# Performance work log

Hardware: AMD Instinct MI355X
Metric: run time of the kernel (lower is better)

Reference implementation:

```python
import jax, jax.numpy as jnp
import numpy as np

B, T, V, E, H, C = 32, 512, 50000, 300, 1024, 2


def setup_inputs() -> dict:
    key = jax.random.key(0)
    ks = jax.random.split(key, 24)
    def w(k, shape):
        return jax.random.normal(k, shape, jnp.float32) * 0.05
    inp = {
        "padded_texts": jax.random.randint(ks[0], (B, T), 0, V),
        "lengths": jax.random.randint(ks[1], (B,), 1, T + 1),
        "emb": w(ks[2], (V, E)),
    }
    i = 3
    for layer, din in ((0, E), (1, 2 * H)):
        for d in ("f", "b"):
            inp[f"w_ih_l{layer}{d}"] = w(ks[i], (4 * H, din)); i += 1
            inp[f"w_hh_l{layer}{d}"] = w(ks[i], (4 * H, H)); i += 1
            inp[f"b_ih_l{layer}{d}"] = w(ks[i], (4 * H,)); i += 1
            inp[f"b_hh_l{layer}{d}"] = w(ks[i], (4 * H,)); i += 1
    inp["lin_w"] = w(ks[i], (C, 2 * H))
    inp["lin_b"] = w(ks[i + 1], (C,))
    return inp


def _reverse_padded(x, lengths):
    # Reverse each sequence within its valid length (pad tail clipped to idx 0;
    # those positions are masked out downstream anyway).
    Tt = x.shape[1]
    idx = jnp.clip(lengths[:, None] - 1 - jnp.arange(Tt)[None, :], 0)
    return jnp.take_along_axis(x, idx[:, :, None], axis=1)


def _run_dir(x, mask, W_ih, W_hh, b_ih, b_hh):
    # x: [B,T,D], mask: [B,T] bool. Returns ([B,T,H] outputs, [B,H] last hidden).
    Bb = x.shape[0]
    Hh = W_hh.shape[1]
    xp = jnp.einsum('btd,gd->btg', x, W_ih) + b_ih + b_hh  # [B,T,4H]
    def step(carry, inp):
        h, c = carry
        g_in, m = inp
        gates = g_in + h @ W_hh.T
        i, f, g, o = jnp.split(gates, 4, axis=-1)  # torch gate order i,f,g,o
        c_new = jax.nn.sigmoid(f) * c + jax.nn.sigmoid(i) * jnp.tanh(g)
        h_new = jax.nn.sigmoid(o) * jnp.tanh(c_new)
        m = m[:, None]
        h = jnp.where(m, h_new, h)
        c = jnp.where(m, c_new, c)
        return (h, c), h
    h0 = jnp.zeros((Bb, Hh), x.dtype)
    (hT, _), outs = jax.lax.scan(step, (h0, h0), (xp.swapaxes(0, 1), mask.T))
    return outs.swapaxes(0, 1), hT


def _bilstm_layer(x, lengths, mask, pf, pb):
    out_f, h_f = _run_dir(x, mask, *pf)
    xr = _reverse_padded(x, lengths)
    out_br, h_b = _run_dir(xr, mask, *pb)
    out_b = _reverse_padded(out_br, lengths)
    return jnp.concatenate([out_f, out_b], -1), h_f, h_b


def reference(padded_texts, lengths, emb,
              w_ih_l0f, w_hh_l0f, b_ih_l0f, b_hh_l0f,
              w_ih_l0b, w_hh_l0b, b_ih_l0b, b_hh_l0b,
              w_ih_l1f, w_hh_l1f, b_ih_l1f, b_hh_l1f,
              w_ih_l1b, w_hh_l1b, b_ih_l1b, b_hh_l1b,
              lin_w, lin_b):
    x = emb[padded_texts]  # [B,T,E]
    mask = jnp.arange(x.shape[1])[None, :] < lengths[:, None]
    x1, _, _ = _bilstm_layer(x, lengths, mask,
                             (w_ih_l0f, w_hh_l0f, b_ih_l0f, b_hh_l0f),
                             (w_ih_l0b, w_hh_l0b, b_ih_l0b, b_hh_l0b))
    _, h2f, h2b = _bilstm_layer(x1, lengths, mask,
                                (w_ih_l1f, w_hh_l1f, b_ih_l1f, b_hh_l1f),
                                (w_ih_l1b, w_hh_l1b, b_ih_l1b, b_hh_l1b))
    # torch: hn[-1] = layer-2 backward, hn[-2] = layer-2 forward;
    # source concatenates (hn[-1], hn[-2]) -> (backward, forward).
    concat = jnp.concatenate([h2b, h2f], axis=1)  # [B,2H]
    return concat @ lin_w.T + lin_b  # [B,2]
```

## Files before the change

### kernel.cpp

```cpp
#include <hip/hip_runtime.h>
#include <hip/hip_bf16.h>
#include <math.h>

typedef __bf16 bf16_8 __attribute__((ext_vector_type(8)));
typedef float  f32x4  __attribute__((ext_vector_type(4)));
typedef unsigned u32x4 __attribute__((ext_vector_type(4)));

#define B_   32
#define T_   512
#define H_   1024
#define G_   4096
#define E_   300
#define EP_  320
#define CT_  128
#define NCH  4

constexpr size_t OFF_HBUF  = 0;
constexpr size_t SZ_ZERO   = 1048576;
constexpr size_t OFF_CBUF  = SZ_ZERO;
constexpr size_t OFF_H2F   = OFF_CBUF + 262144;
constexpr size_t OFF_H2B   = OFF_H2F + 65536;
constexpr size_t OFF_W0F   = OFF_H2B + 65536;
constexpr size_t OFF_W0B   = OFF_W0F + 2621440;
constexpr size_t OFF_W1F   = OFF_W0B + 2621440;
constexpr size_t OFF_W1B   = OFF_W1F + 16777216;
constexpr size_t OFF_EMB   = OFF_W1B + 16777216;
constexpr size_t OFF_OUTF  = OFF_EMB + 32000000;
constexpr size_t OFF_OUTB  = OFF_OUTF + 33554432;
constexpr size_t OFF_XPF   = OFF_OUTB + 33554432;
constexpr size_t OFF_XPB   = OFF_XPF + 33554432;
constexpr size_t WS_NEED   = OFF_XPB + 33554432;

#define WSTR 1032
constexpr int LDS_W  = 0;
constexpr int LDS_H  = 32 * WSTR * 2;
constexpr int LDS_G  = LDS_H + 32 * WSTR * 2;
constexpr int LDS_C  = LDS_G + 32 * 36 * 4;
constexpr int LDS_L  = LDS_C + 32 * 8 * 4;
constexpr int SMEM_REC = LDS_L + 128;

__device__ __forceinline__ float sigf(float x) { return 1.f / (1.f + __expf(-x)); }

__device__ __forceinline__ bf16_8 cvt8(f32x4 lo, f32x4 hi) {
    bf16_8 v;
    #pragma unroll
    for (int e = 0; e < 4; ++e) { v[e] = (__bf16)lo[e]; v[4 + e] = (__bf16)hi[e]; }
    return v;
}

__global__ void pad_w0(const float* __restrict__ wf, const float* __restrict__ wb,
                       __bf16* __restrict__ of, __bf16* __restrict__ ob) {
    int r = blockIdx.x, dir = blockIdx.y, k = threadIdx.x;
    const float* s = dir ? wb : wf;
    __bf16* d = (dir ? ob : of) + (size_t)r * EP_;
    d[k] = (k < E_) ? (__bf16)s[(size_t)r * E_ + k] : (__bf16)0.f;
}

__global__ void cvt_w1(const float* __restrict__ wf, const float* __restrict__ wb,
                       __bf16* __restrict__ of, __bf16* __restrict__ ob) {
    int n = blockIdx.x;
    const float* s = (blockIdx.y ? wb : wf) + (size_t)n * 2048;
    __bf16* d = (blockIdx.y ? ob : of) + (size_t)n * 2048;
    for (int k = threadIdx.x; k < 2048; k += 256) d[k] = (__bf16)s[k];
}

__global__ void cvt_emb(const float* __restrict__ emb, __bf16* __restrict__ embp) {
    int v = blockIdx.x, k = threadIdx.x;
    embp[(size_t)v * EP_ + k] = (k < E_) ? (__bf16)emb[(size_t)v * E_ + k] : (__bf16)0.f;
}

__global__ __launch_bounds__(256) void gemm_l0c(
    const int* __restrict__ texts, const int* __restrict__ lens,
    const __bf16* __restrict__ embp, const __bf16* __restrict__ W,
    const float* __restrict__ bih, const float* __restrict__ bhh,
    __bf16* __restrict__ D, int dir, int t0) {
    constexpr int LDT = 40;
    __shared__ __bf16 As[128 * LDT];
    __shared__ __bf16 Bs[128 * LDT];
    int m0 = (blockIdx.x >> 5) * 128, n0 = (blockIdx.x & 31) * 128;
    int tid = threadIdx.x;
    int rr = tid >> 2, c8 = (tid & 3) * 8;
    const __bf16* pA[2]; const __bf16* pB[2];
    #pragma unroll
    for (int s = 0; s < 2; ++s) {
        int row = m0 + rr + s * 64;
        int b = row >> 7, t = t0 + (row & 127);
        int tt = t;
        if (dir) { int L = lens[b]; tt = L - 1 - t; if (tt < 0) tt = 0; }
        pA[s] = embp + (size_t)texts[b * T_ + tt] * EP_;
        pB[s] = W + (size_t)(n0 + rr + s * 64) * EP_;
    }
    int lane = tid & 63, wid = tid >> 6;
    int wm = (wid >> 1) * 64, wn = (wid & 1) * 64;
    int row16 = lane & 15, quad = lane >> 4;
    bf16_8 apf[2], bpf[2];
    #pragma unroll
    for (int s = 0; s < 2; ++s) {
        apf[s] = *(const bf16_8*)(pA[s] + c8);
        bpf[s] = *(const bf16_8*)(pB[s] + c8);
    }
    f32x4 acc[4][4] = {};
    for (int k0 = 0; k0 < EP_; k0 += 32) {
        #pragma unroll
        for (int s = 0; s < 2; ++s) {
            *(bf16_8*)&As[(rr + s * 64) * LDT + c8] = apf[s];
            *(bf16_8*)&Bs[(rr + s * 64) * LDT + c8] = bpf[s];
        }
        __syncthreads();
        if (k0 + 32 < EP_) {
            int k8 = k0 + 32 + c8;
            #pragma unroll
            for (int s = 0; s < 2; ++s) {
                apf[s] = *(const bf16_8*)(pA[s] + k8);
                bpf[s] = *(const bf16_8*)(pB[s] + k8);
            }
        }
        bf16_8 a[4], b[4];
        #pragma unroll
        for (int i = 0; i < 4; ++i) a[i] = *(const bf16_8*)&As[(wm + i * 16 + row16) * LDT + quad * 8];
        #pragma unroll
        for (int j = 0; j < 4; ++j) b[j] = *(const bf16_8*)&Bs[(wn + j * 16 + row16) * LDT + quad * 8];
        #pragma unroll
        for (int i = 0; i < 4; ++i)
            #pragma unroll
            for (int j = 0; j < 4; ++j)
                acc[i][j] = __builtin_amdgcn_mfma_f32_16x16x32_bf16(a[i], b[j], acc[i][j], 0, 0, 0);
        __syncthreads();
    }
    #pragma unroll
    for (int j = 0; j < 4; ++j) {
        int col = n0 + wn + j * 16 + row16;
        float bias = bih[col] + bhh[col];
        #pragma unroll
        for (int i = 0; i < 4; ++i) {
            int rowb = m0 + wm + i * 16 + quad * 4;
            #pragma unroll
            for (int r = 0; r < 4; ++r)
                D[(size_t)(rowb + r) * G_ + col] = (__bf16)(acc[i][j][r] + bias);
        }
    }
}

__global__ __launch_bounds__(256) void gemm_l1c(
    const __bf16* __restrict__ outf, const __bf16* __restrict__ outbr,
    const int* __restrict__ lens, const __bf16* __restrict__ W,
    const float* __restrict__ bih, const float* __restrict__ bhh,
    __bf16* __restrict__ D, int dir, int t0) {
    constexpr int LDT = 40;
    __shared__ __bf16 As[128 * LDT];
    __shared__ __bf16 Bs[128 * LDT];
    int m0 = (blockIdx.x >> 5) * 128, n0 = (blockIdx.x & 31) * 128;
    int tid = threadIdx.x;
    int rr = tid >> 2, c8 = (tid & 3) * 8;
    const __bf16* pLo[2]; const __bf16* pHi[2]; const __bf16* pB[2];
    #pragma unroll
    for (int s = 0; s < 2; ++s) {
        int row = m0 + rr + s * 64;
        int b = row >> 7, t = t0 + (row & 127);
        int L = lens[b];
        int rev = L - 1 - t; if (rev < 0) rev = 0;
        int tf = dir ? rev : t;
        int tb = dir ? t : rev;
        pLo[s] = outf  + ((size_t)b * T_ + tf) * H_;
        pHi[s] = outbr + ((size_t)b * T_ + tb) * H_;
        pB[s]  = W + (size_t)(n0 + rr + s * 64) * (2 * H_);
    }
    int lane = tid & 63, wid = tid >> 6;
    int wm = (wid >> 1) * 64, wn = (wid & 1) * 64;
    int row16 = lane & 15, quad = lane >> 4;
    bf16_8 apf[2], bpf[2];
    #pragma unroll
    for (int s = 0; s < 2; ++s) {
        apf[s] = *(const bf16_8*)(pLo[s] + c8);
        bpf[s] = *(const bf16_8*)(pB[s] + c8);
    }
    f32x4 acc[4][4] = {};
    for (int k0 = 0; k0 < 2 * H_; k0 += 32) {
        #pragma unroll
        for (int s = 0; s < 2; ++s) {
            *(bf16_8*)&As[(rr + s * 64) * LDT + c8] = apf[s];
            *(bf16_8*)&Bs[(rr + s * 64) * LDT + c8] = bpf[s];
        }
        __syncthreads();
        if (k0 + 32 < 2 * H_) {
            int k8 = k0 + 32 + c8;
            #pragma unroll
            for (int s = 0; s < 2; ++s) {
                const __bf16* src = (k8 < H_) ? pLo[s] + k8 : pHi[s] + (k8 - H_);
                apf[s] = *(const bf16_8*)src;
                bpf[s] = *(const bf16_8*)&pB[s][k8];
            }
        }
        bf16_8 a[4], b[4];
        #pragma unroll
        for (int i = 0; i < 4; ++i) a[i] = *(const bf16_8*)&As[(wm + i * 16 + row16) * LDT + quad * 8];
        #pragma unroll
        for (int j = 0; j < 4; ++j) b[j] = *(const bf16_8*)&Bs[(wn + j * 16 + row16) * LDT + quad * 8];
        #pragma unroll
        for (int i = 0; i < 4; ++i)
            #pragma unroll
            for (int j = 0; j < 4; ++j)
                acc[i][j] = __builtin_amdgcn_mfma_f32_16x16x32_bf16(a[i], b[j], acc[i][j], 0, 0, 0);
        __syncthreads();
    }
    #pragma unroll
    for (int j = 0; j < 4; ++j) {
        int col = n0 + wn + j * 16 + row16;
        float bias = bih[col] + bhh[col];
        #pragma unroll
        for (int i = 0; i < 4; ++i) {
            int rowb = m0 + wm + i * 16 + quad * 4;
            #pragma unroll
            for (int r = 0; r < 4; ++r)
                D[(size_t)(rowb + r) * G_ + col] = (__bf16)(acc[i][j][r] + bias);
        }
    }
}

__global__ __launch_bounds__(256) void lstm_rec(
    const __bf16* __restrict__ xp_f, const __bf16* __restrict__ xp_b,
    const float* __restrict__ whh_f, const float* __restrict__ whh_b,
    const int* __restrict__ lens,
    unsigned* __restrict__ hbuf,
    float* __restrict__ cbuf,
    __bf16* __restrict__ out_f, __bf16* __restrict__ out_b,
    int t0, int seq) {
    extern __shared__ char smem[];
    __bf16* Wl = (__bf16*)(smem + LDS_W);
    __bf16* Hl = (__bf16*)(smem + LDS_H);
    float*  Gl = (float*)(smem + LDS_G);
    float*  Cl = (float*)(smem + LDS_C);
    int*    Ll = (int*)(smem + LDS_L);

    int blk = blockIdx.x;
    int dir = blk >> 7;
    int myb = blk & 127;
    int j0  = myb * 8;
    int tid = threadIdx.x;
    const __bf16* xp  = dir ? xp_b : xp_f;
    const float*  whh = dir ? whh_b : whh_f;
    __bf16* outp = dir ? out_b : out_f;

    int em = tid >> 3, eu = tid & 7;
    int src  = tid & 127;
    int half = tid >> 7;

    for (int i = tid; i < 32 * 128; i += 256) {
        int n = i >> 7, k8 = (i & 127) * 8;
        int grow = (n >> 3) * H_ + j0 + (n & 7);
        f32x4 lo = *(const f32x4*)&whh[(size_t)grow * H_ + k8];
        f32x4 hi = *(const f32x4*)&whh[(size_t)grow * H_ + k8 + 4];
        *(bf16_8*)&Wl[n * WSTR + k8] = cvt8(lo, hi);
    }
    if (tid < 32) Ll[tid] = lens[tid];
    Cl[tid] = (t0 == 0) ? 0.f : cbuf[dir * (B_ * H_) + em * H_ + j0 + eu];
    __syncthreads();

    int lane = tid & 63, wid = tid >> 6;
    int row16 = lane & 15, quad = lane >> 4;
    int m0 = (wid >> 1) * 16, n0 = (wid & 1) * 16;
    int tend = t0 + CT_;

    for (int t = t0; t < tend; ++t) {
        size_t xbase = ((size_t)em * CT_ + (t - t0)) * G_ + j0 + eu;
        __bf16 xg0 = xp[xbase];
        __bf16 xg1 = xp[xbase + H_];
        __bf16 xg2 = xp[xbase + 2 * H_];
        __bf16 xg3 = xp[xbase + 3 * H_];

        const unsigned* hs32 = hbuf + (size_t)((t & 1) * 2 + dir) * (B_ * H_);
        unsigned t16 = (unsigned)t << 16;
        u32x4 tv; tv[0] = t16; tv[1] = t16; tv[2] = t16; tv[3] = t16;
        #pragma unroll 1
        for (int g = 0; g < 2; ++g) {
            u32x4 hv[16];
            while (true) {
                #pragma unroll
                for (int s = 0; s < 8; ++s) {
                    const unsigned* p = hs32 + (half + 2 * (g * 8 + s)) * H_ + src * 8;
                    asm volatile("global_load_dwordx4 %0, %1, off sc0 sc1"
                                 : "=v"(hv[2 * s]) : "v"(p));
                    asm volatile("global_load_dwordx4 %0, %1, off sc0 sc1"
                                 : "=v"(hv[2 * s + 1]) : "v"(p + 4));
                }
                asm volatile("s_waitcnt vmcnt(0)" ::: "memory");
                __builtin_amdgcn_sched_barrier(0);
                u32x4 x = hv[0] ^ tv;
                #pragma unroll
                for (int s = 1; s < 16; ++s) x |= (hv[s] ^ tv);
                if (((x[0] | x[1] | x[2] | x[3]) & 0xffff0000u) == 0) break;
            }
            #pragma unroll
            for (int s = 0; s < 8; ++s) {
                u32x4 lo = hv[2 * s], hi = hv[2 * s + 1], pk;
                pk[0] = (lo[0] & 0xffffu) | (lo[1] << 16);
                pk[1] = (lo[2] & 0xffffu) | (lo[3] << 16);
                pk[2] = (hi[0] & 0xffffu) | (hi[1] << 16);
                pk[3] = (hi[2] & 0xffffu) | (hi[3] << 16);
                *(u32x4*)&Hl[(half + 2 * (g * 8 + s)) * WSTR + src * 8] = pk;
            }
        }
        __syncthreads();
        f32x4 acc0 = {0.f, 0.f, 0.f, 0.f}, acc1 = {0.f, 0.f, 0.f, 0.f};
        #pragma unroll
        for (int kc = 0; kc < 32; kc += 2) {
            bf16_8 a0 = *(const bf16_8*)&Hl[(m0 + row16) * WSTR + kc * 32 + quad * 8];
            bf16_8 b0 = *(const bf16_8*)&Wl[(n0 + row16) * WSTR + kc * 32 + quad * 8];
            acc0 = __builtin_amdgcn_mfma_f32_16x16x32_bf16(a0, b0, acc0, 0, 0, 0);
            bf16_8 a1 = *(const bf16_8*)&Hl[(m0 + row16) * WSTR + (kc + 1) * 32 + quad * 8];
            bf16_8 b1 = *(const bf16_8*)&Wl[(n0 + row16) * WSTR + (kc + 1) * 32 + quad * 8];
            acc1 = __builtin_amdgcn_mfma_f32_16x16x32_bf16(a1, b1, acc1, 0, 0, 0);
        }
        #pragma unroll
        for (int r = 0; r < 4; ++r)
            Gl[(m0 + quad * 4 + r) * 36 + n0 + row16] = acc0[r] + acc1[r];
        __syncthreads();
        {
            float pi = Gl[em * 36 + eu]      + (float)xg0;
            float pf = Gl[em * 36 + 8 + eu]  + (float)xg1;
            float pg = Gl[em * 36 + 16 + eu] + (float)xg2;
            float po = Gl[em * 36 + 24 + eu] + (float)xg3;
            float co = Cl[tid];
            float cn = sigf(pf) * co + sigf(pi) * tanhf(pg);
            float hn = sigf(po) * tanhf(cn);
            __bf16 heff;
            if (t < Ll[em]) { Cl[tid] = cn; heff = (__bf16)hn; }
            else            { heff = Hl[em * WSTR + j0 + eu]; }
            {
                unsigned* hp = hbuf + (size_t)(((t + 1) & 1) * 2 + dir) * (B_ * H_)
                             + em * H_ + j0 + eu;
                unsigned hv32 = ((unsigned)(t + 1) << 16)
                              | (unsigned)*(const unsigned short*)&heff;
                asm volatile("global_store_dword %0, %1, off sc0 sc1"
                             :: "v"(hp), "v"(hv32) : "memory");
            }
            if (seq)              outp[((size_t)em * T_ + t) * H_ + j0 + eu] = heff;
            else if (t == T_ - 1) outp[(size_t)em * H_ + j0 + eu] = heff;
        }
        __syncthreads();
    }
    cbuf[dir * (B_ * H_) + em * H_ + j0 + eu] = Cl[tid];
}

__global__ void final_linear(const __bf16* __restrict__ h2f, const __bf16* __restrict__ h2b,
                             const float* __restrict__ lin_w, const float* __restrict__ lin_b,
                             float* __restrict__ out) {
    __shared__ float red[4];
    int b = blockIdx.x >> 1, c = blockIdx.x & 1;
    int tid = threadIdx.x;
    const __bf16* hb = h2b + (size_t)b * H_;
    const __bf16* hf = h2f + (size_t)b * H_;
    const float* w = lin_w + (size_t)c * (2 * H_);
    float s = 0.f;
    for (int j = tid; j < H_; j += 256)
        s += (float)hb[j] * w[j] + (float)hf[j] * w[H_ + j];
    for (int off = 32; off; off >>= 1) s += __shfl_down(s, off, 64);
    if ((tid & 63) == 0) red[tid >> 6] = s;
    __syncthreads();
    if (tid == 0)
        out[b * 2 + c] = red[0] + red[1] + red[2] + red[3] + lin_b[c];
}

extern "C" void kernel_launch(void* const* d_in, const int* in_sizes, int n_in,
                              void* d_out, int out_size, void* d_ws, size_t ws_size,
                              hipStream_t stream) {
    const int*   texts = (const int*)d_in[0];
    const int*   lens  = (const int*)d_in[1];
    const float* emb   = (const float*)d_in[2];
    const float* wih0f = (const float*)d_in[3];
    const float* whh0f = (const float*)d_in[4];
    const float* bih0f = (const float*)d_in[5];
    const float* bhh0f = (const float*)d_in[6];
    const float* wih0b = (const float*)d_in[7];
    const float* whh0b = (const float*)d_in[8];
    const float* bih0b = (const float*)d_in[9];
    const float* bhh0b = (const float*)d_in[10];
    const float* wih1f = (const float*)d_in[11];
    const float* whh1f = (const float*)d_in[12];
    const float* bih1f = (const float*)d_in[13];
    const float* bhh1f = (const float*)d_in[14];
    const float* wih1b = (const float*)d_in[15];
    const float* whh1b = (const float*)d_in[16];
    const float* bih1b = (const float*)d_in[17];
    const float* bhh1b = (const float*)d_in[18];
    const float* linw  = (const float*)d_in[19];
    const float* linb  = (const float*)d_in[20];

    char* ws = (char*)d_ws;
    unsigned* hbuf  = (unsigned*)(ws + OFF_HBUF);
    float*    cbuf  = (float*)(ws + OFF_CBUF);
    __bf16*   h2f   = (__bf16*)(ws + OFF_H2F);
    __bf16*   h2b   = (__bf16*)(ws + OFF_H2B);
    __bf16*   w0f   = (__bf16*)(ws + OFF_W0F);
    __bf16*   w0b   = (__bf16*)(ws + OFF_W0B);
    __bf16*   w1f   = (__bf16*)(ws + OFF_W1F);
    __bf16*   w1b   = (__bf16*)(ws + OFF_W1B);
    __bf16*   embp  = (__bf16*)(ws + OFF_EMB);
    __bf16*   outf  = (__bf16*)(ws + OFF_OUTF);
    __bf16*   outbr = (__bf16*)(ws + OFF_OUTB);
    __bf16*   xpf   = (__bf16*)(ws + OFF_XPF);
    __bf16*   xpb   = (__bf16*)(ws + OFF_XPB);

    if (ws_size < WS_NEED) return;

    hipMemsetAsync(ws, 0, SZ_ZERO, stream);
    hipFuncSetAttribute((const void*)lstm_rec, hipFuncAttributeMaxDynamicSharedMemorySize, SMEM_REC);

    pad_w0 <<<dim3(G_, 2), 320, 0, stream>>>(wih0f, wih0b, w0f, w0b);
    cvt_w1 <<<dim3(G_, 2), 256, 0, stream>>>(wih1f, wih1b, w1f, w1b);
    cvt_emb<<<50000, 320, 0, stream>>>(emb, embp);

    unsigned* hb0 = hbuf;
    unsigned* hb1 = hbuf + 131072;

    for (int c = 0; c < NCH; ++c) {
        int t0 = c * CT_;
        gemm_l0c<<<1024, 256, 0, stream>>>(texts, lens, embp, w0f, bih0f, bhh0f, xpf, 0, t0);
        gemm_l0c<<<1024, 256, 0, stream>>>(texts, lens, embp, w0b, bih0b, bhh0b, xpb, 1, t0);
        lstm_rec<<<256, 256, SMEM_REC, stream>>>(xpf, xpb, whh0f, whh0b, lens,
                                                 hb0, cbuf, outf, outbr, t0, 1);
    }
    for (int c = 0; c < NCH; ++c) {
        int t0 = c * CT_;
        gemm_l1c<<<1024, 256, 0, stream>>>(outf, outbr, lens, w1f, bih1f, bhh1f, xpf, 0, t0);
        gemm_l1c<<<1024, 256, 0, stream>>>(outf, outbr, lens, w1b, bih1b, bhh1b, xpb, 1, t0);
        lstm_rec<<<256, 256, SMEM_REC, stream>>>(xpf, xpb, whh1f, whh1b, lens,
                                                 hb1, cbuf, h2f, h2b, t0, 0);
    }
    final_linear<<<B_ * 2, 256, 0, stream>>>(h2f, h2b, linw, linb, (float*)d_out);
}
```

Baseline: 6.903 ms.

## Interleave gate columns in xp layout and retry only stale h-buffer chunks

The input-projection GEMMs now write their outputs with the four gate columns of each hidden unit interleaved. This lets the recurrent kernel fetch all four gate preactivations with a single 8-byte vector load per step instead of four scattered 2-byte loads. The h-buffer spin-wait now keeps a per-chunk pending mask, reloading and repacking only chunks whose timestamp tag is still stale rather than re-reading all sixteen vectors on every retry. This reduces memory traffic on the serial critical path, at the cost of a more branchy polling loop.

```diff
diff --git a/kernel.cpp b/kernel.cpp
--- a/kernel.cpp
+++ b/kernel.cpp
@@ -3,6 +3,7 @@
 #include <math.h>
 
 typedef __bf16 bf16_8 __attribute__((ext_vector_type(8)));
+typedef __bf16 bf16_4 __attribute__((ext_vector_type(4)));
 typedef float  f32x4  __attribute__((ext_vector_type(4)));
 typedef unsigned u32x4 __attribute__((ext_vector_type(4)));
 
@@ -131,12 +132,13 @@
     for (int j = 0; j < 4; ++j) {
         int col = n0 + wn + j * 16 + row16;
         float bias = bih[col] + bhh[col];
+        int nc = (col & 1023) * 4 + (col >> 10);
         #pragma unroll
         for (int i = 0; i < 4; ++i) {
             int rowb = m0 + wm + i * 16 + quad * 4;
             #pragma unroll
             for (int r = 0; r < 4; ++r)
-                D[(size_t)(rowb + r) * G_ + col] = (__bf16)(acc[i][j][r] + bias);
+                D[(size_t)(rowb + r) * G_ + nc] = (__bf16)(acc[i][j][r] + bias);
         }
     }
 }
@@ -207,12 +209,13 @@
     for (int j = 0; j < 4; ++j) {
         int col = n0 + wn + j * 16 + row16;
         float bias = bih[col] + bhh[col];
+        int nc = (col & 1023) * 4 + (col >> 10);
         #pragma unroll
         for (int i = 0; i < 4; ++i) {
             int rowb = m0 + wm + i * 16 + quad * 4;
             #pragma unroll
             for (int r = 0; r < 4; ++r)
-                D[(size_t)(rowb + r) * G_ + col] = (__bf16)(acc[i][j][r] + bias);
+                D[(size_t)(rowb + r) * G_ + nc] = (__bf16)(acc[i][j][r] + bias);
         }
     }
 }
@@ -262,43 +265,47 @@
     int tend = t0 + CT_;
 
     for (int t = t0; t < tend; ++t) {
-        size_t xbase = ((size_t)em * CT_ + (t - t0)) * G_ + j0 + eu;
-        __bf16 xg0 = xp[xbase];
-        __bf16 xg1 = xp[xbase + H_];
-        __bf16 xg2 = xp[xbase + 2 * H_];
-        __bf16 xg3 = xp[xbase + 3 * H_];
+        bf16_4 xg = *(const bf16_4*)&xp[((size_t)em * CT_ + (t - t0)) * G_ + (size_t)(j0 + eu) * 4];
 
         const unsigned* hs32 = hbuf + (size_t)((t & 1) * 2 + dir) * (B_ * H_);
         unsigned t16 = (unsigned)t << 16;
-        u32x4 tv; tv[0] = t16; tv[1] = t16; tv[2] = t16; tv[3] = t16;
         #pragma unroll 1
         for (int g = 0; g < 2; ++g) {
             u32x4 hv[16];
-            while (true) {
+            unsigned pend = 0xffu;
+            #pragma unroll 1
+            do {
                 #pragma unroll
-                for (int s = 0; s < 8; ++s) {
-                    const unsigned* p = hs32 + (half + 2 * (g * 8 + s)) * H_ + src * 8;
-                    asm volatile("global_load_dwordx4 %0, %1, off sc0 sc1"
-                                 : "=v"(hv[2 * s]) : "v"(p));
-                    asm volatile("global_load_dwordx4 %0, %1, off sc0 sc1"
-                                 : "=v"(hv[2 * s + 1]) : "v"(p + 4));
+                for (int s2 = 0; s2 < 8; ++s2) {
+                    if (pend & (1u << s2)) {
+                        const unsigned* p = hs32 + (half + 2 * (g * 8 + s2)) * H_ + src * 8;
+                        asm volatile("global_load_dwordx4 %0, %1, off sc0 sc1"
+                                     : "=v"(hv[2 * s2]) : "v"(p));
+                        asm volatile("global_load_dwordx4 %0, %1, off sc0 sc1"
+                                     : "=v"(hv[2 * s2 + 1]) : "v"(p + 4));
+                    }
                 }
                 asm volatile("s_waitcnt vmcnt(0)" ::: "memory");
                 __builtin_amdgcn_sched_barrier(0);
-                u32x4 x = hv[0] ^ tv;
                 #pragma unroll
-                for (int s = 1; s < 16; ++s) x |= (hv[s] ^ tv);
-                if (((x[0] | x[1] | x[2] | x[3]) & 0xffff0000u) == 0) break;
-            }
-            #pragma unroll
-            for (int s = 0; s < 8; ++s) {
-                u32x4 lo = hv[2 * s], hi = hv[2 * s + 1], pk;
-                pk[0] = (lo[0] & 0xffffu) | (lo[1] << 16);
-                pk[1] = (lo[2] & 0xffffu) | (lo[3] << 16);
-                pk[2] = (hi[0] & 0xffffu) | (hi[1] << 16);
-                pk[3] = (hi[2] & 0xffffu) | (hi[3] << 16);
-                *(u32x4*)&Hl[(half + 2 * (g * 8 + s)) * WSTR + src * 8] = pk;
-            }
+                for (int s2 = 0; s2 < 8; ++s2) {
+                    if (pend & (1u << s2)) {
+                        u32x4 lo = hv[2 * s2], hi = hv[2 * s2 + 1];
+                        unsigned bad = ((lo[0] ^ t16) | (lo[1] ^ t16) | (lo[2] ^ t16) | (lo[3] ^ t16)
+                                      | (hi[0] ^ t16) | (hi[1] ^ t16) | (hi[2] ^ t16) | (hi[3] ^ t16))
+                                      & 0xffff0000u;
+                        if (!bad) {
+                            u32x4 pk;
+                            pk[0] = (lo[0] & 0xffffu) | (lo[1] << 16);
+                            pk[1] = (lo[2] & 0xffffu) | (lo[3] << 16);
+                            pk[2] = (hi[0] & 0xffffu) | (hi[1] << 16);
+                            pk[3] = (hi[2] & 0xffffu) | (hi[3] << 16);
+                            *(u32x4*)&Hl[(half + 2 * (g * 8 + s2)) * WSTR + src * 8] = pk;
+                            pend &= ~(1u << s2);
+                        }
+                    }
+                }
+            } while (pend);
         }
         __syncthreads();
         f32x4 acc0 = {0.f, 0.f, 0.f, 0.f}, acc1 = {0.f, 0.f, 0.f, 0.f};
@@ -316,10 +323,10 @@
             Gl[(m0 + quad * 4 + r) * 36 + n0 + row16] = acc0[r] + acc1[r];
         __syncthreads();
         {
-            float pi = Gl[em * 36 + eu]      + (float)xg0;
-            float pf = Gl[em * 36 + 8 + eu]  + (float)xg1;
-            float pg = Gl[em * 36 + 16 + eu] + (float)xg2;
-            float po = Gl[em * 36 + 24 + eu] + (float)xg3;
+            float pi = Gl[em * 36 + eu]      + (float)xg[0];
+            float pf = Gl[em * 36 + 8 + eu]  + (float)xg[1];
+            float pg = Gl[em * 36 + 16 + eu] + (float)xg[2];
+            float po = Gl[em * 36 + 24 + eu] + (float)xg[3];
             float co = Cl[tid];
             float cn = sigf(pf) * co + sigf(pi) * tanhf(pg);
             float hn = sigf(po) * tanhf(cn);
```

Measured after the change: 8.137 ms. +17.9%, slower.
